# Performance work log

Hardware: AMD Instinct MI355X
Metric: run time of the kernel (lower is better)

Reference implementation:

```python
import jax, jax.numpy as jnp
import numpy as np
import math

HEADS = 8
KSIZE = 25  # decomposition moving-average window

def moving_avg(x, k):
    # x: [B, S, E]; replicate-pad last axis by (k-1)//2 on both sides, window mean (stride 1)
    p = (k - 1) // 2
    xp = jnp.pad(x, ((0, 0), (0, 0), (p, p)), mode='edge')
    cs = jnp.cumsum(xp, axis=-1)
    cs = jnp.concatenate([jnp.zeros_like(cs[..., :1]), cs], axis=-1)
    return (cs[..., k:] - cs[..., :-k]) / k

def decompose(x, k):
    trend = moving_avg(x, k)
    return x - trend, trend

def setup_inputs() -> dict:
    key = jax.random.key(0)
    ks = jax.random.split(key, 16)
    B, S, E = 4, 2048, 256
    H = HEADS
    D = E // H
    FF = 4 * E
    OUT = E
    s = 0.02
    inp = {
        'x': jax.random.normal(ks[0], (B, S, E), dtype=jnp.float32),
        'mask': jnp.ones((B, 1, 1, S), dtype=jnp.int32),
        'wq': jax.random.normal(ks[1], (D, D), dtype=jnp.float32) * s,
        'wk': jax.random.normal(ks[2], (D, D), dtype=jnp.float32) * s,
        'wv': jax.random.normal(ks[3], (D, D), dtype=jnp.float32) * s,
        'w_out': jax.random.normal(ks[4], (E, E), dtype=jnp.float32) * s,
        'b_out': jnp.zeros((E,), dtype=jnp.float32),
        'ff_w1': jax.random.normal(ks[5], (E, FF), dtype=jnp.float32) * s,
        'ff_b1': jnp.zeros((FF,), dtype=jnp.float32),
        'ff_w2': jax.random.normal(ks[6], (FF, E), dtype=jnp.float32) * s,
        'ff_b2': jnp.zeros((E,), dtype=jnp.float32),
        'pr_w1': jax.random.normal(ks[7], (E, FF), dtype=jnp.float32) * s,
        'pr_b1': jnp.zeros((FF,), dtype=jnp.float32),
        'pr_w2': jax.random.normal(ks[8], (FF, OUT), dtype=jnp.float32) * s,
        'pr_b2': jnp.zeros((OUT,), dtype=jnp.float32),
    }
    return inp

def reference(x, mask, wq, wk, wv, w_out, b_out, ff_w1, ff_b1, ff_w2, ff_b2, pr_w1, pr_b1, pr_w2, pr_b2):
    B, S, E = x.shape
    H = HEADS
    D = E // H
    # multihead attention (per-head shared projections, scale by sqrt(embed_size))
    xh = x.reshape(B, S, H, D)
    q = xh @ wq
    k = xh @ wk
    v = xh @ wv
    scores = jnp.einsum('nqhd,nkhd->nhqk', q, k) / jnp.float32(math.sqrt(E))
    scores = jnp.where(mask == 0, jnp.float32(-1e20), scores)
    attn = jax.nn.softmax(scores, axis=-1)
    attn_out = jnp.einsum('nhqk,nkhd->nqhd', attn, v).reshape(B, S, E)
    attn_out = attn_out @ w_out + b_out
    # residual (dropout is identity at inference)
    x = x + attn_out
    # first decomposition: keep seasonal part
    y, _ = decompose(x, KSIZE)
    # FFN
    z = jnp.maximum(y @ ff_w1 + ff_b1, 0.0) @ ff_w2 + ff_b2
    s = y + z
    # second decomposition
    s, _ = decompose(s, KSIZE)
    # projection FFN
    out = jnp.maximum(s @ pr_w1 + pr_b1, 0.0) @ pr_w2 + pr_b2
    return out
```

## Files before the change

kernel.cpp:

```cpp
#include <hip/hip_runtime.h>
#include <hip/hip_bf16.h>
#include <math.h>

#define B_   4
#define S_   2048
#define E_   256
#define H_   8
#define D_   32
#define FF_  1024
#define NTOK (B_*S_)

typedef __attribute__((ext_vector_type(8))) short short8;
typedef __attribute__((ext_vector_type(4))) float f32x4;
typedef __attribute__((ext_vector_type(4))) unsigned u32x4;
typedef __hip_bfloat16 bf16;

#define QSCALE 0.09016844005556021f

__device__ __forceinline__ unsigned short round_bf16(float a) {
    unsigned ua = __builtin_bit_cast(unsigned, a);
    return (unsigned short)((ua + 0x7fffu + ((ua >> 16) & 1u)) >> 16);
}
__device__ __forceinline__ unsigned cvtpk_bf16(float lo, float hi) {
    unsigned r;
    asm("v_cvt_pk_bf16_f32 %0, %1, %2" : "=v"(r) : "v"(lo), "v"(hi));
    return r;
}
__device__ __forceinline__ float fexp2(float x) {
    float r;
    asm("v_exp_f32 %0, %1" : "=v"(r) : "v"(x));
    return r;
}
__device__ __forceinline__ void gld16(const short* g, short* l) {
    __builtin_amdgcn_global_load_lds(
        (const __attribute__((address_space(1))) unsigned int*)g,
        (__attribute__((address_space(3))) unsigned int*)l, 16, 0, 0);
}
__device__ __forceinline__ short8 lds_frag(const short* base, int r, int c16) {
    return *(const short8*)(base + r*64 + (((c16) ^ (r & 7)) << 3));
}

__global__ __launch_bounds__(256) void prep_kernel(
    const float* __restrict__ w_out, const float* __restrict__ ff_w1,
    const float* __restrict__ ff_w2, const float* __restrict__ pr_w1,
    const float* __restrict__ pr_w2,
    unsigned short* __restrict__ woT, unsigned short* __restrict__ f1T,
    unsigned short* __restrict__ f2T, unsigned short* __restrict__ p1T,
    unsigned short* __restrict__ p2T,
    const int* __restrict__ mask, int* __restrict__ mflags)
{
    const int bid = blockIdx.x;
    if (bid >= 1088) {
        const int t = threadIdx.x;
        if (t < 128) {
            const int* p = mask + (t >> 5)*S_ + (t & 31)*64;
            int any0 = 0;
            #pragma unroll
            for (int i = 0; i < 16; ++i) {
                const int4 v = *(const int4*)(p + i*4);
                if (!(v.x && v.y && v.z && v.w)) any0 = 1;
            }
            mflags[t] = any0;
        }
        return;
    }
    const float* w; unsigned short* wt; int K, N, idx;
    if (bid < 64)       { w = w_out; wt = woT; K = E_;  N = E_;  idx = bid; }
    else if (bid < 320) { w = ff_w1; wt = f1T; K = E_;  N = FF_; idx = bid - 64; }
    else if (bid < 576) { w = ff_w2; wt = f2T; K = FF_; N = E_;  idx = bid - 320; }
    else if (bid < 832) { w = pr_w1; wt = p1T; K = E_;  N = FF_; idx = bid - 576; }
    else                { w = pr_w2; wt = p2T; K = FF_; N = E_;  idx = bid - 832; }
    const int nb = N/32;
    const int n0 = (idx % nb)*32, k0 = (idx / nb)*32;
    __shared__ float tile[32][33];
    const int c = threadIdx.x & 31, r0 = threadIdx.x >> 5;
    #pragma unroll
    for (int i = 0; i < 4; ++i)
        tile[r0 + 8*i][c] = w[(size_t)(k0 + r0 + 8*i)*N + n0 + c];
    __syncthreads();
    #pragma unroll
    for (int i = 0; i < 4; ++i)
        wt[(size_t)(n0 + r0 + 8*i)*K + k0 + c] = round_bf16(tile[c][r0 + 8*i]);
}

__global__ __launch_bounds__(256) void qkv_kernel(
    const float* __restrict__ x,
    const float* __restrict__ wq, const float* __restrict__ wk, const float* __restrict__ wv,
    bf16* __restrict__ q, bf16* __restrict__ k, bf16* __restrict__ v)
{
    __shared__ float wqs[D_*D_], wks[D_*D_], wvs[D_*D_];
    __shared__ float xs[16][E_];
    const int tid = threadIdx.x;
    for (int i = tid; i < D_*D_; i += 256) {
        wqs[i] = wq[i]; wks[i] = wk[i]; wvs[i] = wv[i];
    }
    const int tok0 = blockIdx.x * 16;
    #pragma unroll
    for (int i = 0; i < 16; ++i)
        xs[i][tid] = x[(size_t)(tok0 + i)*E_ + tid];
    __syncthreads();
    const int h = tid >> 5, d = tid & 31;
    for (int t = 0; t < 16; ++t) {
        float aq = 0.f, ak = 0.f, av = 0.f;
        #pragma unroll
        for (int i = 0; i < D_; ++i) {
            const float xv = xs[t][h*D_ + i];
            aq += xv * wqs[i*D_ + d];
            ak += xv * wks[i*D_ + d];
            av += xv * wvs[i*D_ + d];
        }
        const int tok = tok0 + t;
        const int b = tok >> 11;
        const int s = tok & (S_-1);
        const int u = s & 63;
        const int sp = (s & ~63) | (((u>>5)&1)*32 + ((u>>2)&1)*16 + ((u>>3)&3)*4 + (u&3));
        const size_t base = (size_t)(b*H_ + h)*S_;
        q[(base + s )*D_ + d] = __float2bfloat16(aq * QSCALE);
        k[(base + sp)*D_ + d] = __float2bfloat16(ak);
        v[(base + s )*D_ + d] = __float2bfloat16(av);
    }
}

__global__ __launch_bounds__(256) void vtrans_kernel(
    const short* __restrict__ v, short* __restrict__ vt)
{
    __shared__ short t2[D_][256];
    const int tid = threadIdx.x;
    const int bh = blockIdx.x >> 3;
    const int s0 = (blockIdx.x & 7) * 256;
    const short* src = v + ((size_t)bh*S_ + s0 + tid)*D_;
    const short8 r0 = *(const short8*)(src);
    const short8 r1 = *(const short8*)(src + 8);
    const short8 r2 = *(const short8*)(src + 16);
    const short8 r3 = *(const short8*)(src + 24);
    #pragma unroll
    for (int i = 0; i < 8; ++i) {
        t2[i     ][tid] = r0[i];
        t2[i + 8 ][tid] = r1[i];
        t2[i + 16][tid] = r2[i];
        t2[i + 24][tid] = r3[i];
    }
    __syncthreads();
    const int d = tid >> 3, j = tid & 7;
    short* dst = vt + ((size_t)(bh*D_ + d))*S_ + s0 + j*32;
    const short8* row = (const short8*)&t2[d][j*32];
    const short8 o0 = row[0], o1 = row[1], o2 = row[2], o3 = row[3];
    *(short8*)(dst     ) = o0;
    *(short8*)(dst + 8 ) = o1;
    *(short8*)(dst + 16) = o2;
    *(short8*)(dst + 24) = o3;
}

__global__ __launch_bounds__(256) void attn_mfma_kernel(
    const short* __restrict__ qg, const short* __restrict__ kg,
    const short* __restrict__ vtg, const int* __restrict__ mask,
    const int* __restrict__ mflags, unsigned short* __restrict__ attn_out)
{
    __shared__ alignas(16) short lk[2][64*32];
    __shared__ alignas(16) short lv[2][32*64];

    const int tid  = threadIdx.x;
    const int lane = tid & 63;
    const int wid  = tid >> 6;
    const int c    = lane & 15;
    const int g    = lane >> 4;
    const int p    = ((int)blockIdx.x & 7)*64 + ((int)blockIdx.x >> 3);
    const int bh   = p >> 4;
    const int qt   = p & 15;
    const int b    = bh >> 3;
    const int h    = bh & 7;
    const int q0   = qt*128 + wid*32;

    const short* qrow = qg + ((size_t)bh*S_ + q0 + c)*D_ + g*8;
    const short8 qfA = *(const short8*)(qrow);
    const short8 qfB = *(const short8*)(qrow + 16*D_);
    const short* kbase = kg  + (size_t)bh*S_*D_;
    const short* vbase = vtg + (size_t)bh*D_*S_;
    const int*   mrow  = mask + b*S_;

    const int fl = (lane < 32) ? mflags[b*32 + lane] : 0;
    const unsigned long long mbits = __ballot(fl != 0);

    const short* sbase; int soff0, soff1, sinc, dchunk0;
    if (wid < 2) {
        const int R0 = wid*32 + (lane >> 2);
        const int R1 = R0 + 16;
        const int s  = lane & 3;
        soff0 = R0*D_ + ((s ^ ((R0 >> 1) & 3)) << 3);
        soff1 = R1*D_ + ((s ^ ((R1 >> 1) & 3)) << 3);
        sbase = kbase; sinc = 64*D_;
        dchunk0 = wid*1024;
    } else {
        const int r0 = (wid - 2)*16 + (lane >> 3);
        const int r1 = r0 + 8;
        const int s  = lane & 7;
        soff0 = r0*S_ + ((s ^ (r0 & 7)) << 3);
        soff1 = r1*S_ + ((s ^ (r1 & 7)) << 3);
        sbase = vbase; sinc = 64;
        dchunk0 = (wid - 2)*1024;
    }

    const int kaddr = c*D_ + ((g ^ ((c >> 1) & 3)) << 3);
    const int va0   = c*64 + ((g       ^ (c & 7)) << 3);
    const int va1   = c*64 + (((g + 4) ^ (c & 7)) << 3);
    const f32x4 zero = {0.f,0.f,0.f,0.f};
    f32x4 oA0 = zero, oA1 = zero, oB0 = zero, oB1 = zero;
    float lA = 0.f, lB = 0.f;

    {
        short* d0 = (wid < 2 ? &lk[0][0] : &lv[0][0]) + dchunk0;
        gld16(sbase + soff0, d0);
        gld16(sbase + soff1, d0 + 512);
    }
    __syncthreads();

    int buf = 0;
    for (int t = 0; t < 32; ++t) {
        if (t < 31) {
            const short* sp = sbase + (size_t)(t + 1)*sinc;
            short* d0 = (wid < 2 ? &lk[buf ^ 1][0] : &lv[buf ^ 1][0]) + dchunk0;
            gld16(sp + soff0, d0);
            gld16(sp + soff1, d0 + 512);
        }
        const short* LK = &lk[buf][0];
        const short* LV = &lv[buf][0];
        const short8 kf0 = *(const short8*)(LK + kaddr);
        const short8 kf1 = *(const short8*)(LK + kaddr + 512);
        const short8 kf2 = *(const short8*)(LK + kaddr + 1024);
        const short8 kf3 = *(const short8*)(LK + kaddr + 1536);
        __builtin_amdgcn_s_setprio(1);
        f32x4 sA0 = __builtin_amdgcn_mfma_f32_16x16x32_bf16(kf0, qfA, zero, 0, 0, 0);
        f32x4 sA1 = __builtin_amdgcn_mfma_f32_16x16x32_bf16(kf1, qfA, zero, 0, 0, 0);
        f32x4 sA2 = __builtin_amdgcn_mfma_f32_16x16x32_bf16(kf2, qfA, zero, 0, 0, 0);
        f32x4 sA3 = __builtin_amdgcn_mfma_f32_16x16x32_bf16(kf3, qfA, zero, 0, 0, 0);
        f32x4 sB0 = __builtin_amdgcn_mfma_f32_16x16x32_bf16(kf0, qfB, zero, 0, 0, 0);
        f32x4 sB1 = __builtin_amdgcn_mfma_f32_16x16x32_bf16(kf1, qfB, zero, 0, 0, 0);
        f32x4 sB2 = __builtin_amdgcn_mfma_f32_16x16x32_bf16(kf2, qfB, zero, 0, 0, 0);
        f32x4 sB3 = __builtin_amdgcn_mfma_f32_16x16x32_bf16(kf3, qfB, zero, 0, 0, 0);
        __builtin_amdgcn_s_setprio(0);
        if ((mbits >> t) & 1ull) {
            const int kb = t*64 + 8*g;
            #pragma unroll
            for (int r = 0; r < 4; ++r) {
                if (mrow[kb      + r] == 0) { sA0[r] = -1e20f; sB0[r] = -1e20f; }
                if (mrow[kb + 4  + r] == 0) { sA1[r] = -1e20f; sB1[r] = -1e20f; }
                if (mrow[kb + 32 + r] == 0) { sA2[r] = -1e20f; sB2[r] = -1e20f; }
                if (mrow[kb + 36 + r] == 0) { sA3[r] = -1e20f; sB3[r] = -1e20f; }
            }
        }
        f32x4 pA0, pA1, pA2, pA3, pB0, pB1, pB2, pB3;
        #pragma unroll
        for (int r = 0; r < 4; ++r) {
            pA0[r] = fexp2(sA0[r]); pA1[r] = fexp2(sA1[r]);
            pA2[r] = fexp2(sA2[r]); pA3[r] = fexp2(sA3[r]);
            pB0[r] = fexp2(sB0[r]); pB1[r] = fexp2(sB1[r]);
            pB2[r] = fexp2(sB2[r]); pB3[r] = fexp2(sB3[r]);
        }
        lA += ((pA0[0]+pA0[1])+(pA0[2]+pA0[3])) + ((pA1[0]+pA1[1])+(pA1[2]+pA1[3]))
            + ((pA2[0]+pA2[1])+(pA2[2]+pA2[3])) + ((pA3[0]+pA3[1])+(pA3[2]+pA3[3]));
        lB += ((pB0[0]+pB0[1])+(pB0[2]+pB0[3])) + ((pB1[0]+pB1[1])+(pB1[2]+pB1[3]))
            + ((pB2[0]+pB2[1])+(pB2[2]+pB2[3])) + ((pB3[0]+pB3[1])+(pB3[2]+pB3[3]));
        const short8 pafA0 = __builtin_bit_cast(short8,
            (u32x4){ cvtpk_bf16(pA0[0],pA0[1]), cvtpk_bf16(pA0[2],pA0[3]),
                     cvtpk_bf16(pA1[0],pA1[1]), cvtpk_bf16(pA1[2],pA1[3]) });
        const short8 pafA1 = __builtin_bit_cast(short8,
            (u32x4){ cvtpk_bf16(pA2[0],pA2[1]), cvtpk_bf16(pA2[2],pA2[3]),
                     cvtpk_bf16(pA3[0],pA3[1]), cvtpk_bf16(pA3[2],pA3[3]) });
        const short8 pafB0 = __builtin_bit_cast(short8,
            (u32x4){ cvtpk_bf16(pB0[0],pB0[1]), cvtpk_bf16(pB0[2],pB0[3]),
                     cvtpk_bf16(pB1[0],pB1[1]), cvtpk_bf16(pB1[2],pB1[3]) });
        const short8 pafB1 = __builtin_bit_cast(short8,
            (u32x4){ cvtpk_bf16(pB2[0],pB2[1]), cvtpk_bf16(pB2[2],pB2[3]),
                     cvtpk_bf16(pB3[0],pB3[1]), cvtpk_bf16(pB3[2],pB3[3]) });
        const short8 vf0 = *(const short8*)(LV + va0);
        const short8 vf1 = *(const short8*)(LV + va1);
        const short8 vf2 = *(const short8*)(LV + va0 + 1024);
        const short8 vf3 = *(const short8*)(LV + va1 + 1024);
        __builtin_amdgcn_s_setprio(1);
        oA0 = __builtin_amdgcn_mfma_f32_16x16x32_bf16(vf0, pafA0, oA0, 0, 0, 0);
        oA0 = __builtin_amdgcn_mfma_f32_16x16x32_bf16(vf1, pafA1, oA0, 0, 0, 0);
        oA1 = __builtin_amdgcn_mfma_f32_16x16x32_bf16(vf2, pafA0, oA1, 0, 0, 0);
        oA1 = __builtin_amdgcn_mfma_f32_16x16x32_bf16(vf3, pafA1, oA1, 0, 0, 0);
        oB0 = __builtin_amdgcn_mfma_f32_16x16x32_bf16(vf0, pafB0, oB0, 0, 0, 0);
        oB0 = __builtin_amdgcn_mfma_f32_16x16x32_bf16(vf1, pafB1, oB0, 0, 0, 0);
        oB1 = __builtin_amdgcn_mfma_f32_16x16x32_bf16(vf2, pafB0, oB1, 0, 0, 0);
        oB1 = __builtin_amdgcn_mfma_f32_16x16x32_bf16(vf3, pafB1, oB1, 0, 0, 0);
        __builtin_amdgcn_s_setprio(0);
        __syncthreads();
        buf ^= 1;
    }
    lA += __shfl_xor(lA, 16); lA += __shfl_xor(lA, 32);
    lB += __shfl_xor(lB, 16); lB += __shfl_xor(lB, 32);
    const float invA = 1.0f / lA, invB = 1.0f / lB;
    unsigned short* orowA = attn_out + ((size_t)b*S_ + q0 + c)*E_ + h*D_ + g*4;
    unsigned short* orowB = orowA + (size_t)16*E_;
    uint2 a0, a1, b0, b1;
    a0.x = cvtpk_bf16(oA0[0]*invA, oA0[1]*invA); a0.y = cvtpk_bf16(oA0[2]*invA, oA0[3]*invA);
    a1.x = cvtpk_bf16(oA1[0]*invA, oA1[1]*invA); a1.y = cvtpk_bf16(oA1[2]*invA, oA1[3]*invA);
    b0.x = cvtpk_bf16(oB0[0]*invB, oB0[1]*invB); b0.y = cvtpk_bf16(oB0[2]*invB, oB0[3]*invB);
    b1.x = cvtpk_bf16(oB1[0]*invB, oB1[1]*invB); b1.y = cvtpk_bf16(oB1[2]*invB, oB1[3]*invB);
    *(uint2*)(orowA)      = a0;
    *(uint2*)(orowA + 16) = a1;
    *(uint2*)(orowB)      = b0;
    *(uint2*)(orowB + 16) = b1;
}

template<int BM, int BN, int RELU, int RESID, int WF32, int WBF16>
__global__ __launch_bounds__(256) void mgemm_kernel(
    const short* __restrict__ A, const short* __restrict__ WT,
    const float* __restrict__ bias, const float* __restrict__ R,
    float* __restrict__ C32, unsigned short* __restrict__ Cb,
    int M, int N, int K)
{
    constexpr int FR = BM / 32;
    constexpr int FC = BN / 32;
    __shared__ alignas(16) short As[BM*64];
    __shared__ alignas(16) short Bs[BN*64];
    const int t = threadIdx.x, w = t >> 6, lane = t & 63;
    const int col = lane & 15, grp = lane >> 4;
    const int wm = w >> 1, wn = w & 1;
    const int bm = blockIdx.y, bn = blockIdx.x;
    const int arow = t >> 3, ac = t & 7;

    f32x4 acc[FR][FC];
    #pragma unroll
    for (int i = 0; i < FR; ++i)
        #pragma unroll
        for (int j = 0; j < FC; ++j) acc[i][j] = (f32x4){0.f,0.f,0.f,0.f};

    for (int kb = 0; kb < K; kb += 64) {
        #pragma unroll
        for (int b2 = 0; b2 < BM/32; ++b2) {
            const int row = b2*32 + arow;
            gld16(A + (size_t)(bm*BM + row)*K + kb + ((ac ^ (row & 7)) << 3),
                  As + b2*2048 + w*512);
        }
        #pragma unroll
        for (int b2 = 0; b2 < BN/32; ++b2) {
            const int row = b2*32 + arow;
            gld16(WT + (size_t)(bn*BN + row)*K + kb + ((ac ^ (row & 7)) << 3),
                  Bs + b2*2048 + w*512);
        }
        __syncthreads();
        #pragma unroll
        for (int s = 0; s < 2; ++s) {
            short8 af[FR], bf_[FC];
            #pragma unroll
            for (int fr = 0; fr < FR; ++fr)
                af[fr] = lds_frag(As, wm*(BM/2) + fr*16 + col, s*4 + grp);
            #pragma unroll
            for (int fc = 0; fc < FC; ++fc)
                bf_[fc] = lds_frag(Bs, wn*(BN/2) + fc*16 + col, s*4 + grp);
            #pragma unroll
            for (int fr = 0; fr < FR; ++fr)
                #pragma unroll
                for (int fc = 0; fc < FC; ++fc)
                    acc[fr][fc] = __builtin_amdgcn_mfma_f32_16x16x32_bf16(af[fr], bf_[fc], acc[fr][fc], 0, 0, 0);
        }
        __syncthreads();
    }

    #pragma unroll
    for (int fc = 0; fc < FC; ++fc) {
        const int n = bn*BN + wn*(BN/2) + fc*16 + col;
        const float bs = bias[n];
        #pragma unroll
        for (int fr = 0; fr < FR; ++fr) {
            #pragma unroll
            for (int reg = 0; reg < 4; ++reg) {
                const int m = bm*BM + wm*(BM/2) + fr*16 + grp*4 + reg;
                float v = acc[fr][fc][reg] + bs;
                if (RELU) v = fmaxf(v, 0.f);
                if (RESID) v += R[(size_t)m*N + n];
                if (WF32) C32[(size_t)m*N + n] = v;
                if (WBF16) Cb[(size_t)m*N + n] = round_bf16(v);
            }
        }
    }
}

template<int WF32, int WBF16>
__global__ __launch_bounds__(256) void decomp_kernel(
    const float* __restrict__ in, float* __restrict__ o32, unsigned short* __restrict__ ob)
{
    __shared__ float r[E_];
    const int row = blockIdx.x, e = threadIdx.x;
    const float xv = in[(size_t)row*E_ + e];
    r[e] = xv;
    __syncthreads();
    float sum = 0.f;
    #pragma unroll
    for (int j = -12; j <= 12; ++j) {
        int idx = e + j;
        idx = idx < 0 ? 0 : (idx > E_-1 ? E_-1 : idx);
        sum += r[idx];
    }
    const float res = xv - sum * (1.0f/25.0f);
    if (WF32) o32[(size_t)row*E_ + e] = res;
    if (WBF16) ob[(size_t)row*E_ + e] = round_bf16(res);
}

extern "C" void kernel_launch(void* const* d_in, const int* in_sizes, int n_in,
                              void* d_out, int out_size, void* d_ws, size_t ws_size,
                              hipStream_t stream) {
    const float* x     = (const float*)d_in[0];
    const int*   mask  = (const int*)  d_in[1];
    const float* wq    = (const float*)d_in[2];
    const float* wk    = (const float*)d_in[3];
    const float* wv    = (const float*)d_in[4];
    const float* w_out = (const float*)d_in[5];
    const float* b_out = (const float*)d_in[6];
    const float* ff_w1 = (const float*)d_in[7];
    const float* ff_b1 = (const float*)d_in[8];
    const float* ff_w2 = (const float*)d_in[9];
    const float* ff_b2 = (const float*)d_in[10];
    const float* pr_w1 = (const float*)d_in[11];
    const float* pr_b1 = (const float*)d_in[12];
    const float* pr_w2 = (const float*)d_in[13];
    const float* pr_b2 = (const float*)d_in[14];
    float* out = (float*)d_out;

    char* ws = (char*)d_ws;
    const size_t MB = 1024ull*1024ull;
    const size_t KB = 1024ull;
    bf16*  qb    = (bf16*)(ws + 0*MB);
    bf16*  kbf   = (bf16*)(ws + 4*MB);
    bf16*  vbf   = (bf16*)(ws + 8*MB);
    bf16*  vtb   = (bf16*)(ws + 12*MB);
    unsigned short* attnb = (unsigned short*)(ws + 16*MB);
    float* x1    = (float*)(ws + 20*MB);
    float* y32   = (float*)(ws + 28*MB);
    unsigned short* yb  = (unsigned short*)(ws + 36*MB);
    unsigned short* h1  = (unsigned short*)(ws + 0*MB);
    float* s32   = (float*)(ws + 20*MB);
    unsigned short* s2b = (unsigned short*)(ws + 16*MB);
    unsigned short* h2  = (unsigned short*)(ws + 0*MB);
    unsigned short* woT = (unsigned short*)(ws + 40*MB);
    unsigned short* f1T = (unsigned short*)(ws + 40*MB + 128*KB);
    unsigned short* f2T = (unsigned short*)(ws + 40*MB + 640*KB);
    unsigned short* p1T = (unsigned short*)(ws + 40*MB + 1152*KB);
    unsigned short* p2T = (unsigned short*)(ws + 40*MB + 1664*KB);
    int*            mfl = (int*)           (ws + 40*MB + 2176*KB);

    prep_kernel<<<1089, 256, 0, stream>>>(w_out, ff_w1, ff_w2, pr_w1, pr_w2,
                                          woT, f1T, f2T, p1T, p2T, mask, mfl);
    qkv_kernel<<<NTOK/16, 256, 0, stream>>>(x, wq, wk, wv, qb, kbf, vbf);
    vtrans_kernel<<<B_*H_*(S_/256), 256, 0, stream>>>((const short*)vbf, (short*)vtb);
    attn_mfma_kernel<<<B_*H_*S_/128, 256, 0, stream>>>(
        (const short*)qb, (const short*)kbf, (const short*)vtb, mask, mfl, attnb);
    mgemm_kernel<64,64,0,1,1,0><<<dim3(E_/64, NTOK/64), 256, 0, stream>>>(
        (const short*)attnb, (const short*)woT, b_out, x, x1, nullptr, NTOK, E_, E_);
    decomp_kernel<1,1><<<NTOK, 256, 0, stream>>>(x1, y32, yb);
    mgemm_kernel<128,128,1,0,0,1><<<dim3(FF_/128, NTOK/128), 256, 0, stream>>>(
        (const short*)yb, (const short*)f1T, ff_b1, nullptr, nullptr, h1, NTOK, FF_, E_);
    mgemm_kernel<64,64,0,1,1,0><<<dim3(E_/64, NTOK/64), 256, 0, stream>>>(
        (const short*)h1, (const short*)f2T, ff_b2, y32, s32, nullptr, NTOK, E_, FF_);
    decomp_kernel<0,1><<<NTOK, 256, 0, stream>>>(s32, nullptr, s2b);
    mgemm_kernel<128,128,1,0,0,1><<<dim3(FF_/128, NTOK/128), 256, 0, stream>>>(
        (const short*)s2b, (const short*)p1T, pr_b1, nullptr, nullptr, h2, NTOK, FF_, E_);
    mgemm_kernel<64,64,0,0,1,0><<<dim3(E_/64, NTOK/64), 256, 0, stream>>>(
        (const short*)h2, (const short*)p2T, pr_b2, nullptr, out, nullptr, NTOK, E_, FF_);
}
```

Measured before the change: 129.3 us.

## Merge prep and QKV kernels, MFMA row sums, XCD-aware GEMM block remap

Merges the weight-transpose/mask-flag prep kernel with the QKV projection kernel into one launch, saving a kernel launch and its tail. In attention, the softmax denominators are accumulated with extra MFMAs against a ones vector, using the bf16-rounded probabilities, instead of scalar adds and cross-lane shuffles. GEMM launches switch to a 1D grid with a modulo-8 block remap so neighbouring tiles land on the same XCD for better L2 reuse. The merged kernel now carries the shared memory of both parts, and the MFMA row sum adds matrix-unit work inside the attention inner loop.

```diff
diff --git a/kernel.cpp b/kernel.cpp
--- a/kernel.cpp
+++ b/kernel.cpp
@@ -40,7 +40,10 @@
     return *(const short8*)(base + r*64 + (((c16) ^ (r & 7)) << 3));
 }
 
-__global__ __launch_bounds__(256) void prep_kernel(
+__global__ __launch_bounds__(256) void qkv_prep_kernel(
+    const float* __restrict__ x,
+    const float* __restrict__ wq, const float* __restrict__ wk, const float* __restrict__ wv,
+    bf16* __restrict__ q, bf16* __restrict__ k, bf16* __restrict__ v,
     const float* __restrict__ w_out, const float* __restrict__ ff_w1,
     const float* __restrict__ ff_w2, const float* __restrict__ pr_w1,
     const float* __restrict__ pr_w2,
@@ -50,51 +53,48 @@
     const int* __restrict__ mask, int* __restrict__ mflags)
 {
     const int bid = blockIdx.x;
-    if (bid >= 1088) {
-        const int t = threadIdx.x;
-        if (t < 128) {
-            const int* p = mask + (t >> 5)*S_ + (t & 31)*64;
-            int any0 = 0;
-            #pragma unroll
-            for (int i = 0; i < 16; ++i) {
-                const int4 v = *(const int4*)(p + i*4);
-                if (!(v.x && v.y && v.z && v.w)) any0 = 1;
+    if (bid >= 512) {
+        const int pb = bid - 512;
+        if (pb >= 1088) {
+            const int t = threadIdx.x;
+            if (t < 128) {
+                const int* p = mask + (t >> 5)*S_ + (t & 31)*64;
+                int any0 = 0;
+                #pragma unroll
+                for (int i = 0; i < 16; ++i) {
+                    const int4 vv = *(const int4*)(p + i*4);
+                    if (!(vv.x && vv.y && vv.z && vv.w)) any0 = 1;
+                }
+                mflags[t] = any0;
             }
-            mflags[t] = any0;
-        }
+            return;
+        }
+        const float* w; unsigned short* wt; int K, N, idx;
+        if (pb < 64)       { w = w_out; wt = woT; K = E_;  N = E_;  idx = pb; }
+        else if (pb < 320) { w = ff_w1; wt = f1T; K = E_;  N = FF_; idx = pb - 64; }
+        else if (pb < 576) { w = ff_w2; wt = f2T; K = FF_; N = E_;  idx = pb - 320; }
+        else if (pb < 832) { w = pr_w1; wt = p1T; K = E_;  N = FF_; idx = pb - 576; }
+        else               { w = pr_w2; wt = p2T; K = FF_; N = E_;  idx = pb - 832; }
+        const int nb = N/32;
+        const int n0 = (idx % nb)*32, k0 = (idx / nb)*32;
+        __shared__ float tile[32][33];
+        const int c = threadIdx.x & 31, r0 = threadIdx.x >> 5;
+        #pragma unroll
+        for (int i = 0; i < 4; ++i)
+            tile[r0 + 8*i][c] = w[(size_t)(k0 + r0 + 8*i)*N + n0 + c];
+        __syncthreads();
+        #pragma unroll
+        for (int i = 0; i < 4; ++i)
+            wt[(size_t)(n0 + r0 + 8*i)*K + k0 + c] = round_bf16(tile[c][r0 + 8*i]);
         return;
     }
-    const float* w; unsigned short* wt; int K, N, idx;
-    if (bid < 64)       { w = w_out; wt = woT; K = E_;  N = E_;  idx = bid; }
-    else if (bid < 320) { w = ff_w1; wt = f1T; K = E_;  N = FF_; idx = bid - 64; }
-    else if (bid < 576) { w = ff_w2; wt = f2T; K = FF_; N = E_;  idx = bid - 320; }
-    else if (bid < 832) { w = pr_w1; wt = p1T; K = E_;  N = FF_; idx = bid - 576; }
-    else                { w = pr_w2; wt = p2T; K = FF_; N = E_;  idx = bid - 832; }
-    const int nb = N/32;
-    const int n0 = (idx % nb)*32, k0 = (idx / nb)*32;
-    __shared__ float tile[32][33];
-    const int c = threadIdx.x & 31, r0 = threadIdx.x >> 5;
-    #pragma unroll
-    for (int i = 0; i < 4; ++i)
-        tile[r0 + 8*i][c] = w[(size_t)(k0 + r0 + 8*i)*N + n0 + c];
-    __syncthreads();
-    #pragma unroll
-    for (int i = 0; i < 4; ++i)
-        wt[(size_t)(n0 + r0 + 8*i)*K + k0 + c] = round_bf16(tile[c][r0 + 8*i]);
-}
-
-__global__ __launch_bounds__(256) void qkv_kernel(
-    const float* __restrict__ x,
-    const float* __restrict__ wq, const float* __restrict__ wk, const float* __restrict__ wv,
-    bf16* __restrict__ q, bf16* __restrict__ k, bf16* __restrict__ v)
-{
     __shared__ float wqs[D_*D_], wks[D_*D_], wvs[D_*D_];
     __shared__ float xs[16][E_];
     const int tid = threadIdx.x;
     for (int i = tid; i < D_*D_; i += 256) {
         wqs[i] = wq[i]; wks[i] = wk[i]; wvs[i] = wv[i];
     }
-    const int tok0 = blockIdx.x * 16;
+    const int tok0 = bid * 16;
     #pragma unroll
     for (int i = 0; i < 16; ++i)
         xs[i][tid] = x[(size_t)(tok0 + i)*E_ + tid];
@@ -204,8 +204,10 @@
     const int va0   = c*64 + ((g       ^ (c & 7)) << 3);
     const int va1   = c*64 + (((g + 4) ^ (c & 7)) << 3);
     const f32x4 zero = {0.f,0.f,0.f,0.f};
+    const short8 ones = { (short)0x3F80, (short)0x3F80, (short)0x3F80, (short)0x3F80,
+                          (short)0x3F80, (short)0x3F80, (short)0x3F80, (short)0x3F80 };
     f32x4 oA0 = zero, oA1 = zero, oB0 = zero, oB1 = zero;
-    float lA = 0.f, lB = 0.f;
+    f32x4 lAacc = zero, lBacc = zero;
 
     {
         short* d0 = (wid < 2 ? &lk[0][0] : &lv[0][0]) + dchunk0;
@@ -256,10 +258,6 @@
             pB0[r] = fexp2(sB0[r]); pB1[r] = fexp2(sB1[r]);
             pB2[r] = fexp2(sB2[r]); pB3[r] = fexp2(sB3[r]);
         }
-        lA += ((pA0[0]+pA0[1])+(pA0[2]+pA0[3])) + ((pA1[0]+pA1[1])+(pA1[2]+pA1[3]))
-            + ((pA2[0]+pA2[1])+(pA2[2]+pA2[3])) + ((pA3[0]+pA3[1])+(pA3[2]+pA3[3]));
-        lB += ((pB0[0]+pB0[1])+(pB0[2]+pB0[3])) + ((pB1[0]+pB1[1])+(pB1[2]+pB1[3]))
-            + ((pB2[0]+pB2[1])+(pB2[2]+pB2[3])) + ((pB3[0]+pB3[1])+(pB3[2]+pB3[3]));
         const short8 pafA0 = __builtin_bit_cast(short8,
             (u32x4){ cvtpk_bf16(pA0[0],pA0[1]), cvtpk_bf16(pA0[2],pA0[3]),
                      cvtpk_bf16(pA1[0],pA1[1]), cvtpk_bf16(pA1[2],pA1[3]) });
@@ -285,13 +283,15 @@
         oB0 = __builtin_amdgcn_mfma_f32_16x16x32_bf16(vf1, pafB1, oB0, 0, 0, 0);
         oB1 = __builtin_amdgcn_mfma_f32_16x16x32_bf16(vf2, pafB0, oB1, 0, 0, 0);
         oB1 = __builtin_amdgcn_mfma_f32_16x16x32_bf16(vf3, pafB1, oB1, 0, 0, 0);
+        lAacc = __builtin_amdgcn_mfma_f32_16x16x32_bf16(ones, pafA0, lAacc, 0, 0, 0);
+        lAacc = __builtin_amdgcn_mfma_f32_16x16x32_bf16(ones, pafA1, lAacc, 0, 0, 0);
+        lBacc = __builtin_amdgcn_mfma_f32_16x16x32_bf16(ones, pafB0, lBacc, 0, 0, 0);
+        lBacc = __builtin_amdgcn_mfma_f32_16x16x32_bf16(ones, pafB1, lBacc, 0, 0, 0);
         __builtin_amdgcn_s_setprio(0);
         __syncthreads();
         buf ^= 1;
     }
-    lA += __shfl_xor(lA, 16); lA += __shfl_xor(lA, 32);
-    lB += __shfl_xor(lB, 16); lB += __shfl_xor(lB, 32);
-    const float invA = 1.0f / lA, invB = 1.0f / lB;
+    const float invA = 1.0f / lAacc[0], invB = 1.0f / lBacc[0];
     unsigned short* orowA = attn_out + ((size_t)b*S_ + q0 + c)*E_ + h*D_ + g*4;
     unsigned short* orowB = orowA + (size_t)16*E_;
     uint2 a0, a1, b0, b1;
@@ -319,7 +319,10 @@
     const int t = threadIdx.x, w = t >> 6, lane = t & 63;
     const int col = lane & 15, grp = lane >> 4;
     const int wm = w >> 1, wn = w & 1;
-    const int bm = blockIdx.y, bn = blockIdx.x;
+    const int gx = N / BN;
+    const int nwg = gridDim.x;
+    const int lin = ((int)blockIdx.x & 7)*(nwg >> 3) + ((int)blockIdx.x >> 3);
+    const int bm = lin / gx, bn = lin % gx;
     const int arow = t >> 3, ac = t & 7;
 
     f32x4 acc[FR][FC];
@@ -442,22 +445,22 @@
     unsigned short* p2T = (unsigned short*)(ws + 40*MB + 1664*KB);
     int*            mfl = (int*)           (ws + 40*MB + 2176*KB);
 
-    prep_kernel<<<1089, 256, 0, stream>>>(w_out, ff_w1, ff_w2, pr_w1, pr_w2,
-                                          woT, f1T, f2T, p1T, p2T, mask, mfl);
-    qkv_kernel<<<NTOK/16, 256, 0, stream>>>(x, wq, wk, wv, qb, kbf, vbf);
+    qkv_prep_kernel<<<1601, 256, 0, stream>>>(x, wq, wk, wv, qb, kbf, vbf,
+                                              w_out, ff_w1, ff_w2, pr_w1, pr_w2,
+                                              woT, f1T, f2T, p1T, p2T, mask, mfl);
     vtrans_kernel<<<B_*H_*(S_/256), 256, 0, stream>>>((const short*)vbf, (short*)vtb);
     attn_mfma_kernel<<<B_*H_*S_/128, 256, 0, stream>>>(
         (const short*)qb, (const short*)kbf, (const short*)vtb, mask, mfl, attnb);
-    mgemm_kernel<64,64,0,1,1,0><<<dim3(E_/64, NTOK/64), 256, 0, stream>>>(
+    mgemm_kernel<64,64,0,1,1,0><<<(NTOK/64)*(E_/64), 256, 0, stream>>>(
         (const short*)attnb, (const short*)woT, b_out, x, x1, nullptr, NTOK, E_, E_);
     decomp_kernel<1,1><<<NTOK, 256, 0, stream>>>(x1, y32, yb);
-    mgemm_kernel<128,128,1,0,0,1><<<dim3(FF_/128, NTOK/128), 256, 0, stream>>>(
+    mgemm_kernel<128,128,1,0,0,1><<<(NTOK/128)*(FF_/128), 256, 0, stream>>>(
         (const short*)yb, (const short*)f1T, ff_b1, nullptr, nullptr, h1, NTOK, FF_, E_);
-    mgemm_kernel<64,64,0,1,1,0><<<dim3(E_/64, NTOK/64), 256, 0, stream>>>(
+    mgemm_kernel<64,64,0,1,1,0><<<(NTOK/64)*(E_/64), 256, 0, stream>>>(
         (const short*)h1, (const short*)f2T, ff_b2, y32, s32, nullptr, NTOK, E_, FF_);
     decomp_kernel<0,1><<<NTOK, 256, 0, stream>>>(s32, nullptr, s2b);
-    mgemm_kernel<128,128,1,0,0,1><<<dim3(FF_/128, NTOK/128), 256, 0, stream>>>(
+    mgemm_kernel<128,128,1,0,0,1><<<(NTOK/128)*(FF_/128), 256, 0, stream>>>(
         (const short*)s2b, (const short*)p1T, pr_b1, nullptr, nullptr, h2, NTOK, FF_, E_);
-    mgemm_kernel<64,64,0,0,1,0><<<dim3(E_/64, NTOK/64), 256, 0, stream>>>(
+    mgemm_kernel<64,64,0,0,1,0><<<(NTOK/64)*(E_/64), 256, 0, stream>>>(
         (const short*)h2, (const short*)p2T, pr_b2, nullptr, out, nullptr, NTOK, E_, FF_);
 }
```

New measurement: 125.3 us. 1.03x faster.
